# Kernel optimization log

Measured on AMD Instinct MI355X. Metric: run time of the kernel, lower is better.

Reference implementation:

```python
import jax, jax.numpy as jnp
import numpy as np

EPS = 1e-6  # VNLeakyReLU eps
NORM_EPS = 1e-12  # F.normalize default eps
NEG_SLOPE = 0.2


def _normalize(v):
    # matches torch F.normalize(p=2, dim=-1): v / max(||v||, eps)
    n = jnp.linalg.norm(v, axis=-1, keepdims=True)
    return v / jnp.maximum(n, NORM_EPS)


def _bgs_extended(d6s):
    # d6s: [B,N,D,3,2] -> rotation matrices [B,N,D,3,3] (columns b1,b2,b3)
    b1 = _normalize(d6s[..., 0])
    a2 = d6s[..., 1]
    proj = jnp.sum(b1 * a2, axis=-1, keepdims=True) * b1
    b2 = _normalize(a2 - proj)
    b3 = jnp.cross(b1, b2)
    return jnp.stack([b1, b2, b3], axis=-1)


def setup_inputs() -> dict:
    key = jax.random.key(0)
    kX, kJ, kA, kB, kC, kW = jax.random.split(key, 6)
    B, N, Din, Dout = 8, 4096, 128, 256
    return {
        "X": jax.random.normal(kX, (B, N, Din, 3), dtype=jnp.float32),
        "J": jax.random.normal(kJ, (B, N, Din, 3, 2), dtype=jnp.float32),
        "Amat": jax.random.normal(kA, (Dout, Din), dtype=jnp.float32),
        "Bmat": jax.random.normal(kB, (Dout, Din), dtype=jnp.float32),
        "Cmat": jax.random.normal(kC, (Dout, Din), dtype=jnp.float32),
        "Wdir": jax.random.normal(kW, (Dout, Dout), dtype=jnp.float32),
        "device": 0,
    }


def reference(X, J, Amat, Bmat, Cmat, Wdir, device):
    # ---- Affine_Linear_Abla_wocomplex ----
    R = _bgs_extended(J)  # [B,N,D,3,3]
    # get_rtx(k, RT, X) = sum_j R[...,j,k] * X[...,j]; stacking k=0,1,2 gives:
    a_term = jnp.einsum('bndjk,bndj->bndk', R, X)  # [B,N,D,3]
    # Y = A@a + B@a + C@a == (A+B+C)@a  (einsum 'fe,bcei->bcfi')
    Y = jnp.einsum('fe,bnei->bnfi', Amat + Bmat + Cmat, a_term)  # [B,N,F,3]
    # ---- permute(0,2,3,1) -> [B, F, 3, N] ----
    x = jnp.transpose(Y, (0, 2, 3, 1))
    # ---- VNLeakyReLU ----
    d = jnp.einsum('oc,bcin->boin', Wdir, x)
    dot = jnp.sum(x * d, axis=2, keepdims=True)
    mask = (dot >= 0).astype(x.dtype)
    d_norm_sq = jnp.sum(d * d, axis=2, keepdims=True)
    x_out = NEG_SLOPE * x + (1 - NEG_SLOPE) * (
        mask * x + (1 - mask) * (x - dot / (d_norm_sq + EPS) * d)
    )
    return x_out  # [B, F, 3, N]
```

## Files before the change

kernel.cpp:

```cpp
#include <hip/hip_runtime.h>

#define TT 16
#define NBLK 2048
#define LDA 136
#define LDY 264

typedef short s16x8 __attribute__((ext_vector_type(8)));
typedef float f32x4 __attribute__((ext_vector_type(4)));

#define SCHED_FENCE() __builtin_amdgcn_sched_barrier(0)

__device__ __forceinline__ unsigned short f2bf(float f) {
  union { float f; unsigned u; } v; v.f = f;
  unsigned r = v.u + 0x7FFFu + ((v.u >> 16) & 1u);
  return (unsigned short)(r >> 16);
}
__device__ __forceinline__ float bf2f(unsigned short h) {
  union { unsigned u; float f; } v; v.u = ((unsigned)h) << 16;
  return v.f;
}
__device__ __forceinline__ void split2(float x, unsigned short& h, unsigned short& m) {
  h = f2bf(x);
  m = f2bf(x - bf2f(h));
}

__global__ __launch_bounds__(256) void prep_kernel(
    const float* __restrict__ A, const float* __restrict__ Bm,
    const float* __restrict__ C, const float* __restrict__ W,
    unsigned short* __restrict__ M3h, unsigned short* __restrict__ M3m,
    unsigned short* __restrict__ Wh, unsigned short* __restrict__ Wm) {
  int tid = blockIdx.x * 256 + threadIdx.x;
  if (tid < 128 * 256) {
    unsigned short h, m;
    split2(A[tid] + Bm[tid] + C[tid], h, m);
    M3h[tid] = h; M3m[tid] = m;
  } else {
    int t2 = tid - 128 * 256;
    unsigned short h, m;
    split2(W[t2], h, m);
    Wh[t2] = h; Wm[t2] = m;
  }
}

#define B1LOAD(ks) { \
  b1h[ks][0] = *(const s16x8*)(M3h + fB1 + (ks) * 32); \
  b1m[ks][0] = *(const s16x8*)(M3m + fB1 + (ks) * 32); \
  b1h[ks][1] = *(const s16x8*)(M3h + fB1 + 2048 + (ks) * 32); \
  b1m[ks][1] = *(const s16x8*)(M3m + fB1 + 2048 + (ks) * 32); }

#define W2LOAD(ks) { \
  w2h[ks][0] = *(const s16x8*)(Wh + fB2 + (ks) * 32); \
  w2m[ks][0] = *(const s16x8*)(Wm + fB2 + (ks) * 32); \
  w2h[ks][1] = *(const s16x8*)(Wh + fB2 + 4096 + (ks) * 32); \
  w2m[ks][1] = *(const s16x8*)(Wm + fB2 + 4096 + (ks) * 32); }

#define G1STEP(ks) { \
  const int e0 = (ks) * 32 + quad * 8; \
  _Pragma("unroll") \
  for (int mt = 0; mt < 3; ++mt) { \
    s16x8 ah = *(const s16x8*)(aTh + (mt * 16 + nl) * LDA + e0); \
    s16x8 am = *(const s16x8*)(aTm + (mt * 16 + nl) * LDA + e0); \
    _Pragma("unroll") \
    for (int nt = 0; nt < 2; ++nt) { \
      f32x4 a = acc1[mt][nt]; \
      a = __builtin_amdgcn_mfma_f32_16x16x32_bf16(ah, b1h[ks][nt], a, 0, 0, 0); \
      a = __builtin_amdgcn_mfma_f32_16x16x32_bf16(ah, b1m[ks][nt], a, 0, 0, 0); \
      a = __builtin_amdgcn_mfma_f32_16x16x32_bf16(am, b1h[ks][nt], a, 0, 0, 0); \
      acc1[mt][nt] = a; \
    } \
  } }

#define G2STEP(ks) { \
  const int c0 = (ks) * 32 + quad * 8; \
  _Pragma("unroll") \
  for (int mt = 0; mt < 3; ++mt) { \
    s16x8 ah = *(const s16x8*)(Yth + (mt * 16 + nl) * LDY + c0); \
    s16x8 am = *(const s16x8*)(Ytm + (mt * 16 + nl) * LDY + c0); \
    _Pragma("unroll") \
    for (int nt = 0; nt < 2; ++nt) { \
      f32x4 a = acc2[mt][nt]; \
      a = __builtin_amdgcn_mfma_f32_16x16x32_bf16(ah, w2h[ks][nt], a, 0, 0, 0); \
      a = __builtin_amdgcn_mfma_f32_16x16x32_bf16(ah, w2m[ks][nt], a, 0, 0, 0); \
      a = __builtin_amdgcn_mfma_f32_16x16x32_bf16(am, w2h[ks][nt], a, 0, 0, 0); \
      acc2[mt][nt] = a; \
    } \
  } }

__global__ __launch_bounds__(512, 4) void affine_vnrelu_mfma(
    const float* __restrict__ X, const float* __restrict__ J,
    const unsigned short* __restrict__ M3h, const unsigned short* __restrict__ M3m,
    const unsigned short* __restrict__ Wh, const unsigned short* __restrict__ Wm,
    float* __restrict__ out) {
  __shared__ unsigned short smem[2 * 48 * LDA + 2 * 48 * LDY];
  unsigned short* aTh = smem;
  unsigned short* aTm = smem + 48 * LDA;
  unsigned short* Yth = smem + 2 * 48 * LDA;
  unsigned short* Ytm = Yth + 48 * LDY;

  const int tid = threadIdx.x;
  const int lane = tid & 63;
  const int w = tid >> 6;
  const int quad = lane >> 4;
  const int nl = lane & 15;
  const long g0 = (long)blockIdx.x * TT;
  const int b = (int)(g0 >> 12);
  const int n0 = (int)(g0 & 4095);
  const int f0 = w * 32;
  const int fB1 = (f0 + nl) * 128 + quad * 8;
  const int fB2 = (f0 + nl) * 256 + quad * 8;
  const f32x4 zz = {0.f, 0.f, 0.f, 0.f};

  s16x8 b1h[4][2], b1m[4][2];
  B1LOAD(0); B1LOAD(1);
  SCHED_FENCE();

  {
    int t = tid >> 5;
    int dch0 = (tid & 31) * 4;
    const float* Xp = X + ((g0 + t) * 128 + dch0) * 3;
    const float* Jp = J + ((g0 + t) * 128 + dch0) * 6;
    float xf[12], jf[24];
    #pragma unroll
    for (int q = 0; q < 3; ++q) *(float4*)(xf + 4 * q) = ((const float4*)Xp)[q];
    #pragma unroll
    for (int q = 0; q < 6; ++q) *(float4*)(jf + 4 * q) = ((const float4*)Jp)[q];

    unsigned short hs[3][4], ms[3][4];
    #pragma unroll
    for (int e = 0; e < 4; ++e) {
      float x0 = xf[3 * e], x1 = xf[3 * e + 1], x2 = xf[3 * e + 2];
      float j0 = jf[6 * e],     j1 = jf[6 * e + 1], j2 = jf[6 * e + 2];
      float j3 = jf[6 * e + 3], j4 = jf[6 * e + 4], j5 = jf[6 * e + 5];
      float c00 = j0, c01 = j2, c02 = j4;
      float a20 = j1, a21 = j3, a22 = j5;
      float nsq1 = c00 * c00 + c01 * c01 + c02 * c02;
      float inv1 = __builtin_amdgcn_rsqf(fmaxf(nsq1, 1e-24f));
      float b10 = c00 * inv1, b11 = c01 * inv1, b12 = c02 * inv1;
      float pr = b10 * a20 + b11 * a21 + b12 * a22;
      float u0 = a20 - pr * b10, u1 = a21 - pr * b11, u2 = a22 - pr * b12;
      float nsq2 = u0 * u0 + u1 * u1 + u2 * u2;
      float inv2 = __builtin_amdgcn_rsqf(fmaxf(nsq2, 1e-24f));
      float b20 = u0 * inv2, b21 = u1 * inv2, b22 = u2 * inv2;
      float b30 = b11 * b22 - b12 * b21;
      float b31 = b12 * b20 - b10 * b22;
      float b32 = b10 * b21 - b11 * b20;
      split2(b10 * x0 + b11 * x1 + b12 * x2, hs[0][e], ms[0][e]);
      split2(b20 * x0 + b21 * x1 + b22 * x2, hs[1][e], ms[1][e]);
      split2(b30 * x0 + b31 * x1 + b32 * x2, hs[2][e], ms[2][e]);
    }
    #pragma unroll
    for (int i = 0; i < 3; ++i) {
      short4 vh, vm;
      vh.x = hs[i][0]; vh.y = hs[i][1]; vh.z = hs[i][2]; vh.w = hs[i][3];
      vm.x = ms[i][0]; vm.y = ms[i][1]; vm.z = ms[i][2]; vm.w = ms[i][3];
      int ro = (i * 16 + t) * LDA + dch0;
      *(short4*)(aTh + ro) = vh;
      *(short4*)(aTm + ro) = vm;
    }
  }
  __syncthreads();

  f32x4 acc1[3][2];
  #pragma unroll
  for (int mt = 0; mt < 3; ++mt)
    #pragma unroll
    for (int nt = 0; nt < 2; ++nt) acc1[mt][nt] = zz;

  B1LOAD(2); B1LOAD(3);
  SCHED_FENCE();
  G1STEP(0);
  G1STEP(1);
  G1STEP(2);
  G1STEP(3);

  s16x8 w2h[8][2], w2m[8][2];
  W2LOAD(0); W2LOAD(1);
  SCHED_FENCE();

  #pragma unroll
  for (int mt = 0; mt < 3; ++mt)
    #pragma unroll
    for (int nt = 0; nt < 2; ++nt)
      #pragma unroll
      for (int r = 0; r < 4; ++r) {
        unsigned short h, m;
        split2(acc1[mt][nt][r], h, m);
        int yo = (mt * 16 + quad * 4 + r) * LDY + f0 + nt * 16 + nl;
        Yth[yo] = h; Ytm[yo] = m;
      }
  __syncthreads();

  f32x4 acc2[3][2];
  #pragma unroll
  for (int mt = 0; mt < 3; ++mt)
    #pragma unroll
    for (int nt = 0; nt < 2; ++nt) acc2[mt][nt] = zz;

  W2LOAD(2); W2LOAD(3);
  SCHED_FENCE();
  G2STEP(0);
  SCHED_FENCE();
  W2LOAD(4);
  SCHED_FENCE();
  G2STEP(1);
  SCHED_FENCE();
  W2LOAD(5);
  SCHED_FENCE();
  G2STEP(2);
  SCHED_FENCE();
  W2LOAD(6);
  SCHED_FENCE();
  G2STEP(3);
  SCHED_FENCE();
  W2LOAD(7);
  SCHED_FENCE();
  G2STEP(4);
  G2STEP(5);
  G2STEP(6);
  G2STEP(7);

  #pragma unroll
  for (int nt = 0; nt < 2; ++nt) {
    int f = f0 + nt * 16 + nl;
    float* ob = out + ((long)(b * 256 + f) * 3) * 4096 + n0 + quad * 4;
    float o[3][4];
    #pragma unroll
    for (int r = 0; r < 4; ++r) {
      int row = quad * 4 + r;
      float x0 = bf2f(Yth[row * LDY + f])        + bf2f(Ytm[row * LDY + f]);
      float x1 = bf2f(Yth[(16 + row) * LDY + f]) + bf2f(Ytm[(16 + row) * LDY + f]);
      float x2 = bf2f(Yth[(32 + row) * LDY + f]) + bf2f(Ytm[(32 + row) * LDY + f]);
      float d0 = acc2[0][nt][r], d1 = acc2[1][nt][r], d2 = acc2[2][nt][r];
      float dot = x0 * d0 + x1 * d1 + x2 * d2;
      float dn = d0 * d0 + d1 * d1 + d2 * d2;
      float s = (dot < 0.0f) ? (0.8f * dot * __builtin_amdgcn_rcpf(dn + 1e-6f))
                             : 0.0f;
      o[0][r] = x0 - s * d0;
      o[1][r] = x1 - s * d1;
      o[2][r] = x2 - s * d2;
    }
    #pragma unroll
    for (int i = 0; i < 3; ++i)
      *(float4*)(ob + ((long)i * 4096)) = make_float4(o[i][0], o[i][1], o[i][2], o[i][3]);
  }
}

extern "C" void kernel_launch(void* const* d_in, const int* in_sizes, int n_in,
                              void* d_out, int out_size, void* d_ws, size_t ws_size,
                              hipStream_t stream) {
  const float* X = (const float*)d_in[0];
  const float* J = (const float*)d_in[1];
  const float* A = (const float*)d_in[2];
  const float* B = (const float*)d_in[3];
  const float* C = (const float*)d_in[4];
  const float* W = (const float*)d_in[5];
  unsigned short* M3h = (unsigned short*)d_ws;
  unsigned short* M3m = M3h + 128 * 256;
  unsigned short* Wh  = M3m + 128 * 256;
  unsigned short* Wm  = Wh + 256 * 256;
  float* out = (float*)d_out;

  prep_kernel<<<(128 * 256 + 256 * 256) / 256, 256, 0, stream>>>(
      A, B, C, W, M3h, M3m, Wh, Wm);
  affine_vnrelu_mfma<<<NBLK, 512, 0, stream>>>(
      X, J, M3h, M3m, Wh, Wm, out);
}
```

Baseline: 291.1 us.

## Fold Wdir into combined weight so second GEMM reads a_term directly

Precomputes WM = Wdir·(A+B+C) in a new prep kernel, so the direction vector d is computed from the rotated input a_term (K=128) instead of from Y (K=256). This halves the second GEMM's reduction length and removes the Y split/store to shared memory, a __syncthreads, and the shared buffer for Y. x is now taken directly from the fp32 accumulators. The cost is an extra small prep launch and a slightly different rounding path, since d no longer sees the bf16 rounding of Y.

```diff
diff --git a/kernel.cpp b/kernel.cpp
--- a/kernel.cpp
+++ b/kernel.cpp
@@ -3,7 +3,6 @@
 #define TT 16
 #define NBLK 2048
 #define LDA 136
-#define LDY 264
 
 typedef short s16x8 __attribute__((ext_vector_type(8)));
 typedef float f32x4 __attribute__((ext_vector_type(4)));
@@ -24,35 +23,47 @@
   m = f2bf(x - bf2f(h));
 }
 
-__global__ __launch_bounds__(256) void prep_kernel(
+__global__ __launch_bounds__(256) void prep1_kernel(
     const float* __restrict__ A, const float* __restrict__ Bm,
-    const float* __restrict__ C, const float* __restrict__ W,
-    unsigned short* __restrict__ M3h, unsigned short* __restrict__ M3m,
-    unsigned short* __restrict__ Wh, unsigned short* __restrict__ Wm) {
+    const float* __restrict__ C,
+    float* __restrict__ M3f,
+    unsigned short* __restrict__ M3h, unsigned short* __restrict__ M3m) {
   int tid = blockIdx.x * 256 + threadIdx.x;
-  if (tid < 128 * 256) {
-    unsigned short h, m;
-    split2(A[tid] + Bm[tid] + C[tid], h, m);
-    M3h[tid] = h; M3m[tid] = m;
-  } else {
-    int t2 = tid - 128 * 256;
-    unsigned short h, m;
-    split2(W[t2], h, m);
-    Wh[t2] = h; Wm[t2] = m;
-  }
+  float s = A[tid] + Bm[tid] + C[tid];
+  M3f[tid] = s;
+  unsigned short h, m;
+  split2(s, h, m);
+  M3h[tid] = h; M3m[tid] = m;
+}
+
+__global__ __launch_bounds__(128) void prep2_kernel(
+    const float* __restrict__ W, const float* __restrict__ M3f,
+    unsigned short* __restrict__ WMh, unsigned short* __restrict__ WMm) {
+  __shared__ float wrow[256];
+  const int o = blockIdx.x;
+  const int e = threadIdx.x;
+  wrow[e]       = W[o * 256 + e];
+  wrow[e + 128] = W[o * 256 + 128 + e];
+  __syncthreads();
+  float dot = 0.f;
+  #pragma unroll 8
+  for (int c = 0; c < 256; ++c) dot += wrow[c] * M3f[c * 128 + e];
+  unsigned short h, m;
+  split2(dot, h, m);
+  WMh[o * 128 + e] = h; WMm[o * 128 + e] = m;
 }
 
 #define B1LOAD(ks) { \
-  b1h[ks][0] = *(const s16x8*)(M3h + fB1 + (ks) * 32); \
-  b1m[ks][0] = *(const s16x8*)(M3m + fB1 + (ks) * 32); \
-  b1h[ks][1] = *(const s16x8*)(M3h + fB1 + 2048 + (ks) * 32); \
-  b1m[ks][1] = *(const s16x8*)(M3m + fB1 + 2048 + (ks) * 32); }
-
-#define W2LOAD(ks) { \
-  w2h[ks][0] = *(const s16x8*)(Wh + fB2 + (ks) * 32); \
-  w2m[ks][0] = *(const s16x8*)(Wm + fB2 + (ks) * 32); \
-  w2h[ks][1] = *(const s16x8*)(Wh + fB2 + 4096 + (ks) * 32); \
-  w2m[ks][1] = *(const s16x8*)(Wm + fB2 + 4096 + (ks) * 32); }
+  b1h[ks][0] = *(const s16x8*)(M3h + fB + (ks) * 32); \
+  b1m[ks][0] = *(const s16x8*)(M3m + fB + (ks) * 32); \
+  b1h[ks][1] = *(const s16x8*)(M3h + fB + 2048 + (ks) * 32); \
+  b1m[ks][1] = *(const s16x8*)(M3m + fB + 2048 + (ks) * 32); }
+
+#define WMLOAD(ks) { \
+  wmh[ks][0] = *(const s16x8*)(WMh + fB + (ks) * 32); \
+  wmm[ks][0] = *(const s16x8*)(WMm + fB + (ks) * 32); \
+  wmh[ks][1] = *(const s16x8*)(WMh + fB + 2048 + (ks) * 32); \
+  wmm[ks][1] = *(const s16x8*)(WMm + fB + 2048 + (ks) * 32); }
 
 #define G1STEP(ks) { \
   const int e0 = (ks) * 32 + quad * 8; \
@@ -71,17 +82,17 @@
   } }
 
 #define G2STEP(ks) { \
-  const int c0 = (ks) * 32 + quad * 8; \
+  const int e0 = (ks) * 32 + quad * 8; \
   _Pragma("unroll") \
   for (int mt = 0; mt < 3; ++mt) { \
-    s16x8 ah = *(const s16x8*)(Yth + (mt * 16 + nl) * LDY + c0); \
-    s16x8 am = *(const s16x8*)(Ytm + (mt * 16 + nl) * LDY + c0); \
+    s16x8 ah = *(const s16x8*)(aTh + (mt * 16 + nl) * LDA + e0); \
+    s16x8 am = *(const s16x8*)(aTm + (mt * 16 + nl) * LDA + e0); \
     _Pragma("unroll") \
     for (int nt = 0; nt < 2; ++nt) { \
       f32x4 a = acc2[mt][nt]; \
-      a = __builtin_amdgcn_mfma_f32_16x16x32_bf16(ah, w2h[ks][nt], a, 0, 0, 0); \
-      a = __builtin_amdgcn_mfma_f32_16x16x32_bf16(ah, w2m[ks][nt], a, 0, 0, 0); \
-      a = __builtin_amdgcn_mfma_f32_16x16x32_bf16(am, w2h[ks][nt], a, 0, 0, 0); \
+      a = __builtin_amdgcn_mfma_f32_16x16x32_bf16(ah, wmh[ks][nt], a, 0, 0, 0); \
+      a = __builtin_amdgcn_mfma_f32_16x16x32_bf16(ah, wmm[ks][nt], a, 0, 0, 0); \
+      a = __builtin_amdgcn_mfma_f32_16x16x32_bf16(am, wmh[ks][nt], a, 0, 0, 0); \
       acc2[mt][nt] = a; \
     } \
   } }
@@ -89,13 +100,11 @@
 __global__ __launch_bounds__(512, 4) void affine_vnrelu_mfma(
     const float* __restrict__ X, const float* __restrict__ J,
     const unsigned short* __restrict__ M3h, const unsigned short* __restrict__ M3m,
-    const unsigned short* __restrict__ Wh, const unsigned short* __restrict__ Wm,
+    const unsigned short* __restrict__ WMh, const unsigned short* __restrict__ WMm,
     float* __restrict__ out) {
-  __shared__ unsigned short smem[2 * 48 * LDA + 2 * 48 * LDY];
+  __shared__ unsigned short smem[2 * 48 * LDA];
   unsigned short* aTh = smem;
   unsigned short* aTm = smem + 48 * LDA;
-  unsigned short* Yth = smem + 2 * 48 * LDA;
-  unsigned short* Ytm = Yth + 48 * LDY;
 
   const int tid = threadIdx.x;
   const int lane = tid & 63;
@@ -106,12 +115,12 @@
   const int b = (int)(g0 >> 12);
   const int n0 = (int)(g0 & 4095);
   const int f0 = w * 32;
-  const int fB1 = (f0 + nl) * 128 + quad * 8;
-  const int fB2 = (f0 + nl) * 256 + quad * 8;
+  const int fB = (f0 + nl) * 128 + quad * 8;
   const f32x4 zz = {0.f, 0.f, 0.f, 0.f};
 
   s16x8 b1h[4][2], b1m[4][2];
-  B1LOAD(0); B1LOAD(1);
+  s16x8 wmh[4][2], wmm[4][2];
+  B1LOAD(0);
   SCHED_FENCE();
 
   {
@@ -166,29 +175,18 @@
     #pragma unroll
     for (int nt = 0; nt < 2; ++nt) acc1[mt][nt] = zz;
 
-  B1LOAD(2); B1LOAD(3);
+  B1LOAD(1);
   SCHED_FENCE();
   G1STEP(0);
+  B1LOAD(2);
+  SCHED_FENCE();
   G1STEP(1);
+  B1LOAD(3);
+  SCHED_FENCE();
   G1STEP(2);
+  WMLOAD(0); WMLOAD(1);
+  SCHED_FENCE();
   G1STEP(3);
-
-  s16x8 w2h[8][2], w2m[8][2];
-  W2LOAD(0); W2LOAD(1);
-  SCHED_FENCE();
-
-  #pragma unroll
-  for (int mt = 0; mt < 3; ++mt)
-    #pragma unroll
-    for (int nt = 0; nt < 2; ++nt)
-      #pragma unroll
-      for (int r = 0; r < 4; ++r) {
-        unsigned short h, m;
-        split2(acc1[mt][nt][r], h, m);
-        int yo = (mt * 16 + quad * 4 + r) * LDY + f0 + nt * 16 + nl;
-        Yth[yo] = h; Ytm[yo] = m;
-      }
-  __syncthreads();
 
   f32x4 acc2[3][2];
   #pragma unroll
@@ -196,28 +194,14 @@
     #pragma unroll
     for (int nt = 0; nt < 2; ++nt) acc2[mt][nt] = zz;
 
-  W2LOAD(2); W2LOAD(3);
-  SCHED_FENCE();
   G2STEP(0);
-  SCHED_FENCE();
-  W2LOAD(4);
+  WMLOAD(2);
   SCHED_FENCE();
   G2STEP(1);
-  SCHED_FENCE();
-  W2LOAD(5);
+  WMLOAD(3);
   SCHED_FENCE();
   G2STEP(2);
-  SCHED_FENCE();
-  W2LOAD(6);
-  SCHED_FENCE();
   G2STEP(3);
-  SCHED_FENCE();
-  W2LOAD(7);
-  SCHED_FENCE();
-  G2STEP(4);
-  G2STEP(5);
-  G2STEP(6);
-  G2STEP(7);
 
   #pragma unroll
   for (int nt = 0; nt < 2; ++nt) {
@@ -226,10 +210,7 @@
     float o[3][4];
     #pragma unroll
     for (int r = 0; r < 4; ++r) {
-      int row = quad * 4 + r;
-      float x0 = bf2f(Yth[row * LDY + f])        + bf2f(Ytm[row * LDY + f]);
-      float x1 = bf2f(Yth[(16 + row) * LDY + f]) + bf2f(Ytm[(16 + row) * LDY + f]);
-      float x2 = bf2f(Yth[(32 + row) * LDY + f]) + bf2f(Ytm[(32 + row) * LDY + f]);
+      float x0 = acc1[0][nt][r], x1 = acc1[1][nt][r], x2 = acc1[2][nt][r];
       float d0 = acc2[0][nt][r], d1 = acc2[1][nt][r], d2 = acc2[2][nt][r];
       float dot = x0 * d0 + x1 * d1 + x2 * d2;
       float dn = d0 * d0 + d1 * d1 + d2 * d2;
@@ -256,12 +237,13 @@
   const float* W = (const float*)d_in[5];
   unsigned short* M3h = (unsigned short*)d_ws;
   unsigned short* M3m = M3h + 128 * 256;
-  unsigned short* Wh  = M3m + 128 * 256;
-  unsigned short* Wm  = Wh + 256 * 256;
+  unsigned short* WMh = M3m + 128 * 256;
+  unsigned short* WMm = WMh + 128 * 256;
+  float* M3f = (float*)(WMm + 128 * 256);
   float* out = (float*)d_out;
 
-  prep_kernel<<<(128 * 256 + 256 * 256) / 256, 256, 0, stream>>>(
-      A, B, C, W, M3h, M3m, Wh, Wm);
+  prep1_kernel<<<128, 256, 0, stream>>>(A, B, C, M3f, M3h, M3m);
+  prep2_kernel<<<256, 128, 0, stream>>>(W, M3f, WMh, WMm);
   affine_vnrelu_mfma<<<NBLK, 512, 0, stream>>>(
-      X, J, M3h, M3m, Wh, Wm, out);
-}
+      X, J, M3h, M3m, WMh, WMm, out);
+}
```

Result: faster. 280.7 us (-3.6%).
